# Kernel tuning notes

Measured on AMD Instinct MI355X. Metric: run time of the kernel, lower is better.

Reference implementation:

```python
import jax, jax.numpy as jnp
import numpy as np

HIDDEN = 4096
N_HEADS = 32
HEAD_DIM = HIDDEN // N_HEADS  # 128
ROPE_BASE = 10000.0


def _rotate_half(x):
    h = x.shape[-1] // 2
    return jnp.concatenate((-x[..., h:], x[..., :h]), axis=-1)


def _rope_sin_cos(position_ids):
    # position_ids: [B, S] int -> sin, cos: [B, 1, S, head_dim]
    inv_freq = 1.0 / (ROPE_BASE ** (jnp.arange(0, HEAD_DIM, 2, dtype=jnp.float32) / HEAD_DIM))
    freqs = position_ids.astype(jnp.float32)[..., None] * inv_freq  # [B,S,hd/2]
    emb = jnp.concatenate((freqs, freqs), axis=-1)  # [B,S,hd]
    return jnp.sin(emb)[:, None, :, :], jnp.cos(emb)[:, None, :, :]


def setup_inputs() -> dict:
    key = jax.random.key(0)
    k1, k2, k3 = jax.random.split(key, 3)
    B, S = 2, 2048
    hidden_states = jax.random.normal(k1, (B, S, HIDDEN), dtype=jnp.float32)
    w_qkv = jax.random.normal(k2, (HIDDEN, 3 * HIDDEN), dtype=jnp.float32) * 0.02
    wo = jax.random.normal(k3, (HIDDEN, HIDDEN), dtype=jnp.float32) * 0.02
    position_ids = jnp.broadcast_to(jnp.arange(S, dtype=jnp.int32)[None, :], (B, S))
    return {"hidden_states": hidden_states, "w_qkv": w_qkv, "wo": wo,
            "position_ids": position_ids}


def reference(hidden_states, w_qkv, wo, position_ids):
    B, S, H = hidden_states.shape
    qkv = hidden_states @ w_qkv  # [B,S,3H]
    q, k, v = jnp.split(qkv, 3, axis=-1)
    # [B,S,nH,hd] -> [B,nH,S,hd]
    q = q.reshape(B, S, N_HEADS, HEAD_DIM).transpose(0, 2, 1, 3)
    k = k.reshape(B, S, N_HEADS, HEAD_DIM).transpose(0, 2, 1, 3)
    v = v.reshape(B, S, N_HEADS, HEAD_DIM).transpose(0, 2, 1, 3)
    sin, cos = _rope_sin_cos(position_ids)  # [B,1,S,hd]
    q = q * cos + _rotate_half(q) * sin
    k = k * cos + _rotate_half(k) * sin
    scale = 1.0 / np.sqrt(HEAD_DIM)
    scores = jnp.einsum('bhqd,bhkd->bhqk', q, k) * scale
    causal = jnp.tril(jnp.ones((S, S), dtype=bool))
    scores = jnp.where(causal[None, None, :, :], scores, jnp.finfo(scores.dtype).min)
    attn = jax.nn.softmax(scores, axis=-1)
    out = jnp.einsum('bhqk,bhkd->bhqd', attn, v)  # [B,nH,S,hd]
    out = out.transpose(0, 2, 1, 3).reshape(B, S, H)
    return out @ wo
```

## Files before the change

kernel.cpp:

```cpp
#include <hip/hip_runtime.h>

typedef unsigned int u32;
typedef unsigned short u16;
typedef short short8 __attribute__((ext_vector_type(8)));
typedef float f32x4 __attribute__((ext_vector_type(4)));
typedef unsigned short us4 __attribute__((ext_vector_type(4)));

#define S_LEN 2048
#define BATCH 2
#define HID 4096
#define NH 32
#define HD 128
#define TRIH 12288

#define GCAST(p) ((const __attribute__((address_space(1))) u32*)(p))
#define LCAST(p) ((__attribute__((address_space(3))) u32*)(p))

static __device__ __forceinline__ u16 f2bf(float f) {
  union { float f; u32 u; } x; x.f = f;
  u32 u = x.u;
  u32 r = u + 0x7FFFu + ((u >> 16) & 1u);
  return (u16)(r >> 16);
}
static __device__ __forceinline__ float bf2f(u16 h) {
  union { u32 u; float f; } x; x.u = ((u32)h) << 16;
  return x.f;
}

__global__ __launch_bounds__(256) void cvt_f32_bf16(const float* __restrict__ in,
                                                    u16* __restrict__ out, int n4) {
  int i = blockIdx.x * 256 + threadIdx.x;
  if (i >= n4) return;
  float4 v = ((const float4*)in)[i];
  us4 o;
  o.x = f2bf(v.x); o.y = f2bf(v.y); o.z = f2bf(v.z); o.w = f2bf(v.w);
  ((us4*)out)[i] = o;
}

__global__ __launch_bounds__(256) void tr_cvt(const float* __restrict__ in,
                                              u16* __restrict__ out, int R, int C) {
  __shared__ float tile[64][65];
  int c0 = blockIdx.x * 64, r0 = blockIdx.y * 64;
  int tx = threadIdx.x;
  int rr = tx >> 4;
  int cc = (tx & 15) << 2;
#pragma unroll
  for (int it = 0; it < 4; ++it) {
    float4 v = *(const float4*)&in[(size_t)(r0 + rr + it * 16) * C + c0 + cc];
    tile[rr + it * 16][cc + 0] = v.x;
    tile[rr + it * 16][cc + 1] = v.y;
    tile[rr + it * 16][cc + 2] = v.z;
    tile[rr + it * 16][cc + 3] = v.w;
  }
  __syncthreads();
#pragma unroll
  for (int it = 0; it < 4; ++it) {
    int crow = rr + it * 16;
    us4 o;
    o.x = f2bf(tile[cc + 0][crow]);
    o.y = f2bf(tile[cc + 1][crow]);
    o.z = f2bf(tile[cc + 2][crow]);
    o.w = f2bf(tile[cc + 3][crow]);
    *(us4*)&out[(size_t)(c0 + crow) * R + r0 + cc] = o;
  }
}


template<int MQ, int NQ>
static __device__ __forceinline__ void mfma_quad(f32x4 (&acc)[8][4], short8 (&af)[4][2],
                                                 short8 (&bfr)[4][2]) {
#pragma unroll
  for (int ml = 0; ml < 4; ++ml)
#pragma unroll
    for (int nl = 0; nl < 2; ++nl) {
      acc[MQ*4+ml][NQ*2+nl] = __builtin_amdgcn_mfma_f32_16x16x32_bf16(
          af[ml][0], bfr[NQ*2+nl][0], acc[MQ*4+ml][NQ*2+nl], 0, 0, 0);
      acc[MQ*4+ml][NQ*2+nl] = __builtin_amdgcn_mfma_f32_16x16x32_bf16(
          af[ml][1], bfr[NQ*2+nl][1], acc[MQ*4+ml][NQ*2+nl], 0, 0, 0);
    }
}

template<int MQ>
static __device__ __forceinline__ void read_a(short8 (&af)[4][2], const u16* abase, int lane) {
#pragma unroll
  for (int ml = 0; ml < 4; ++ml) {
    int r = MQ*64 + ml*16 + (lane & 15);
#pragma unroll
    for (int kh = 0; kh < 2; ++kh) {
      int j = kh*4 + (lane >> 4);
      af[ml][kh] = *(const short8*)(abase + r*64 + ((j ^ (r & 7)) << 3));
    }
  }
}
template<int NQ>
static __device__ __forceinline__ void read_b(short8 (&bfr)[4][2], const u16* bbase,
                                              int rbase, int lane) {
#pragma unroll
  for (int nl = 0; nl < 2; ++nl) {
    int r = rbase + (NQ*2+nl)*16 + (lane & 15);
#pragma unroll
    for (int kh = 0; kh < 2; ++kh) {
      int j = kh*4 + (lane >> 4);
      bfr[NQ*2+nl][kh] = *(const short8*)(bbase + r*64 + ((j ^ (r & 7)) << 3));
    }
  }
}

#define SEAM_CLOSE0() \
  asm volatile("s_waitcnt vmcnt(0)" ::: "memory"); \
  __builtin_amdgcn_s_barrier(); \
  __builtin_amdgcn_sched_barrier(0);

template<int OUTF32>
__global__ __launch_bounds__(512, 1) void gemm256(const u16* __restrict__ A,
                                                  const u16* __restrict__ Bt,
                                                  void* __restrict__ Cout,
                                                  int M, int N, int K, int nbm) {
  __shared__ __attribute__((aligned(16))) u16 lds[65536];
  const int tid = threadIdx.x, wave = tid >> 6, lane = tid & 63;
  const int wr = wave >> 2, wc = wave & 3;
  const int nwg = gridDim.x, wg = blockIdx.x, cpx = nwg >> 3;
  const int swz = (wg & 7) * cpx + (wg >> 3);
  const size_t tileM = (size_t)(swz % nbm) * 256;
  const size_t tileN = (size_t)(swz / nbm) * 256;
  const int nIter = K >> 7;

  const int r_ = tid >> 3;
  const int gc_ = (tid & 7) ^ (r_ & 7);

  const u16* Ag = A + tileM * K;
  const u16* Bg = Bt + tileN * K;

  f32x4 acc[8][4] = {};
  short8 af[4][2], bfr[4][2];

  auto stageA = [&](int kt, int buf, int half) {
    const u16* g0 = Ag + (size_t)(half*128 + r_) * K + kt*64 + (gc_ << 3);
    u16* l = lds + buf*16384 + half*8192 + wave*512;
    __builtin_amdgcn_global_load_lds(GCAST(g0), LCAST(l), 16, 0, 0);
    __builtin_amdgcn_global_load_lds(GCAST(g0 + (size_t)64*K), LCAST(l + 4096), 16, 0, 0);
  };
  auto stageB = [&](int kt, int buf, int half) {
    const u16* g0 = Bg + (size_t)(half*128 + r_) * K + kt*64 + (gc_ << 3);
    u16* l = lds + 32768 + buf*16384 + half*8192 + wave*512;
    __builtin_amdgcn_global_load_lds(GCAST(g0), LCAST(l), 16, 0, 0);
    __builtin_amdgcn_global_load_lds(GCAST(g0 + (size_t)64*K), LCAST(l + 4096), 16, 0, 0);
  };

  const u16* a0 = lds + wr*8192;
  const u16* a1 = lds + 16384 + wr*8192;
  const u16* b0 = lds + 32768 + (wc >> 1)*8192;
  const u16* b1 = lds + 32768 + 16384 + (wc >> 1)*8192;
  const int brb = (wc & 1) * 64;

  stageA(0, 0, 0); stageA(0, 0, 1);
  stageB(0, 0, 0); stageB(0, 0, 1);
  SEAM_CLOSE0()

  for (int i = 0; i < nIter; ++i) {
    const int t1 = 2*i + 1, t2 = 2*i + 2;
    const bool more = (i + 1 < nIter);

    read_a<0>(af, a0, lane);
    read_b<0>(bfr, b0, brb, lane);
    read_b<1>(bfr, b0, brb, lane);
    stageA(t1, 1, 0); stageA(t1, 1, 1);
    stageB(t1, 1, 0); stageB(t1, 1, 1);
    mfma_quad<0, 0>(acc, af, bfr);
    mfma_quad<0, 1>(acc, af, bfr);
    read_a<1>(af, a0, lane);
    mfma_quad<1, 0>(acc, af, bfr);
    mfma_quad<1, 1>(acc, af, bfr);
    SEAM_CLOSE0()

    read_a<0>(af, a1, lane);
    read_b<0>(bfr, b1, brb, lane);
    read_b<1>(bfr, b1, brb, lane);
    if (more) { stageA(t2, 0, 0); stageA(t2, 0, 1); stageB(t2, 0, 0); stageB(t2, 0, 1); }
    mfma_quad<0, 0>(acc, af, bfr);
    mfma_quad<0, 1>(acc, af, bfr);
    read_a<1>(af, a1, lane);
    mfma_quad<1, 0>(acc, af, bfr);
    mfma_quad<1, 1>(acc, af, bfr);
    if (more) { SEAM_CLOSE0() }
  }

  const int r0o = (lane >> 4) << 2, c0o = lane & 15;
#pragma unroll
  for (int m = 0; m < 8; ++m)
#pragma unroll
    for (int n = 0; n < 4; ++n)
#pragma unroll
      for (int rr = 0; rr < 4; ++rr) {
        size_t grow = tileM + wr*128 + m*16 + r0o + rr;
        size_t gcol = tileN + wc*64 + n*16 + c0o;
        if (OUTF32) ((float*)Cout)[grow * N + gcol] = acc[m][n][rr];
        else        ((u16*)Cout)[grow * N + gcol] = f2bf(acc[m][n][rr]);
      }
}

__global__ __launch_bounds__(256) void rope_kernel(u16* __restrict__ qkv,
                                                   const int* __restrict__ pid) {
  int idx = blockIdx.x * 256 + threadIdx.x;
  int row = idx >> 9;
  int rem = idx & 511;
  int which = rem >> 8;
  int h = (rem >> 3) & 31;
  int j0 = (rem & 7) << 3;
  u16* p = qkv + (size_t)row * TRIH + which * HID + h * HD + j0;
  short8 lo = *(short8*)p;
  short8 hi = *(short8*)(p + 64);
  float pos = (float)pid[row];
  short8 olo, ohi;
#pragma unroll
  for (int i = 0; i < 8; ++i) {
    float x0 = bf2f((u16)lo[i]), x1 = bf2f((u16)hi[i]);
    float th = pos * expf(-(float)(j0 + i) * 0.14391156831212787f);
    float sn, cs;
    sincosf(th, &sn, &cs);
    olo[i] = (short)f2bf(x0 * cs - x1 * sn);
    ohi[i] = (short)f2bf(x1 * cs + x0 * sn);
  }
  *(short8*)p = olo;
  *(short8*)(p + 64) = ohi;
}

__global__ __launch_bounds__(512, 2) void attn_kernel(const u16* __restrict__ qkv,
                                                      u16* __restrict__ O) {
  const int bid = blockIdx.x;
  const int qt = 15 - (bid >> 6);
  const int bh = bid & 63;
  const int b = bh >> 5, h = bh & 31;
  const int tid = threadIdx.x, wave = tid >> 6, lane = tid & 63;
  __shared__ u16 Ks[2][64 * 128];
  __shared__ u16 VsT[2][128 * 64];
  __shared__ u16 Ps[8][16 * 64];
  const u16* base = qkv + (size_t)b * S_LEN * TRIH + h * HD;

  const int rbase = (lane >> 4) << 2;
  const int cbase = lane & 15;
  const int q_lo = qt * 128;
  const int wrow0 = q_lo + wave * 16;

  short8 qf[4];
  {
    const u16* qrow = base + (size_t)(wrow0 + cbase) * TRIH;
#pragma unroll
    for (int f = 0; f < 4; ++f)
      qf[f] = *(const short8*)(qrow + ((f * 4 + (lane >> 4)) << 3));
  }

  const int tmax_w = 2 * qt + (wave >= 4 ? 1 : 0);
  const int tmax_b = 2 * qt + 1;

  float mrun[4], lrun[4];
  f32x4 accO[8] = {};
#pragma unroll
  for (int r = 0; r < 4; ++r) { mrun[r] = -1e30f; lrun[r] = 0.f; }

  short8 kreg[2], vreg[2];
  auto load_tile = [&](int t) {
    int kv = t << 6;
#pragma unroll
    for (int it = 0; it < 2; ++it) {
      int c = tid + it * 512;
      int row = c >> 4, ch = c & 15;
      const u16* src = base + (size_t)(kv + row) * TRIH + (ch << 3);
      kreg[it] = *(const short8*)(src + HID);
      vreg[it] = *(const short8*)(src + 2 * HID);
    }
  };
  auto write_tile = [&](int buf) {
#pragma unroll
    for (int it = 0; it < 2; ++it) {
      int c = tid + it * 512;
      int row = c >> 4, ch = c & 15;
      *(short8*)(Ks[buf] + row * 128 + ((ch ^ (row & 7)) << 3)) = kreg[it];
#pragma unroll
      for (int i = 0; i < 8; ++i) {
        int d = (ch << 3) + i;
        VsT[buf][d * 64 + (((row >> 3) ^ (ch & 7)) << 3) + (row & 7)] = (u16)vreg[it][i];
      }
    }
  };

  load_tile(0);
  write_tile(0);
  load_tile(1);

  for (int t = 0; t <= tmax_b; ++t) {
    const int cur = t & 1;
    __syncthreads();
    if (t < tmax_b) write_tile(cur ^ 1);
    if (t + 2 <= tmax_b) load_tile(t + 2);

    if (t > tmax_w) continue;

    f32x4 s[4] = {};
#pragma unroll
    for (int n = 0; n < 4; ++n) {
      int krow = n * 16 + cbase;
#pragma unroll
      for (int f = 0; f < 4; ++f) {
        int ch = f * 4 + (lane >> 4);
        short8 kf = *(const short8*)(Ks[cur] + krow * 128 + ((ch ^ (krow & 7)) << 3));
        s[n] = __builtin_amdgcn_mfma_f32_16x16x32_bf16(qf[f], kf, s[n], 0, 0, 0);
      }
    }
    const float scale = 0.08838834764831845f;
    const int kv0 = t << 6;
    if (t == tmax_w) {
#pragma unroll
      for (int n = 0; n < 4; ++n)
#pragma unroll
        for (int r = 0; r < 4; ++r) {
          int kvcol = kv0 + n * 16 + cbase;
          int qrow = wrow0 + rbase + r;
          s[n][r] = (kvcol <= qrow) ? s[n][r] * scale : -1e30f;
        }
    } else {
#pragma unroll
      for (int n = 0; n < 4; ++n) s[n] *= scale;
    }

    float tmax[4];
#pragma unroll
    for (int r = 0; r < 4; ++r) {
      float tm = fmaxf(fmaxf(s[0][r], s[1][r]), fmaxf(s[2][r], s[3][r]));
      tm = fmaxf(tm, __shfl_xor(tm, 1));
      tm = fmaxf(tm, __shfl_xor(tm, 2));
      tm = fmaxf(tm, __shfl_xor(tm, 4));
      tm = fmaxf(tm, __shfl_xor(tm, 8));
      tmax[r] = tm;
    }
    bool need = false;
#pragma unroll
    for (int r = 0; r < 4; ++r) need |= (tmax[r] > mrun[r] + 8.0f);
    if (__any(need)) {
#pragma unroll
      for (int r = 0; r < 4; ++r) {
        float mnew = fmaxf(mrun[r], tmax[r]);
        float corr = __expf(mrun[r] - mnew);
        float rs = 0.f;
#pragma unroll
        for (int n = 0; n < 4; ++n) { float pv = __expf(s[n][r] - mnew); s[n][r] = pv; rs += pv; }
        rs += __shfl_xor(rs, 1); rs += __shfl_xor(rs, 2);
        rs += __shfl_xor(rs, 4); rs += __shfl_xor(rs, 8);
        lrun[r] = lrun[r] * corr + rs;
        mrun[r] = mnew;
#pragma unroll
        for (int nd = 0; nd < 8; ++nd) accO[nd][r] *= corr;
      }
    } else {
#pragma unroll
      for (int r = 0; r < 4; ++r) {
        float rs = 0.f;
#pragma unroll
        for (int n = 0; n < 4; ++n) { float pv = __expf(s[n][r] - mrun[r]); s[n][r] = pv; rs += pv; }
        rs += __shfl_xor(rs, 1); rs += __shfl_xor(rs, 2);
        rs += __shfl_xor(rs, 4); rs += __shfl_xor(rs, 8);
        lrun[r] += rs;
      }
    }

    u16* Pw = (u16*)Ps[wave];
#pragma unroll
    for (int n = 0; n < 4; ++n)
#pragma unroll
      for (int r = 0; r < 4; ++r) {
        int rl = rbase + r;
        int col = n * 16 + cbase;
        Pw[rl * 64 + (((col >> 3) ^ (rl & 7)) << 3) + (col & 7)] = f2bf(s[n][r]);
      }

    short8 pa[2];
    {
      int prow = lane & 15;
#pragma unroll
      for (int f2 = 0; f2 < 2; ++f2) {
        int ch = f2 * 4 + (lane >> 4);
        pa[f2] = *(const short8*)(Pw + prow * 64 + ((ch ^ (prow & 7)) << 3));
      }
    }
#pragma unroll
    for (int nd = 0; nd < 8; ++nd) {
      int drow = nd * 16 + cbase;
#pragma unroll
      for (int f2 = 0; f2 < 2; ++f2) {
        int ch = f2 * 4 + (lane >> 4);
        short8 vb = *(const short8*)(VsT[cur] + drow * 64 + ((ch ^ ((drow >> 3) & 7)) << 3));
        accO[nd] = __builtin_amdgcn_mfma_f32_16x16x32_bf16(pa[f2], vb, accO[nd], 0, 0, 0);
      }
    }
  }

#pragma unroll
  for (int nd = 0; nd < 8; ++nd)
#pragma unroll
    for (int r = 0; r < 4; ++r) {
      int qrow = wrow0 + rbase + r;
      int col = h * HD + nd * 16 + cbase;
      O[(size_t)(b * S_LEN + qrow) * HID + col] = f2bf(accO[nd][r] / lrun[r]);
    }
}

extern "C" void kernel_launch(void* const* d_in, const int* in_sizes, int n_in,
                              void* d_out, int out_size, void* d_ws, size_t ws_size,
                              hipStream_t stream) {
  const float* hidden = (const float*)d_in[0];
  const float* w_qkv  = (const float*)d_in[1];
  const float* wo     = (const float*)d_in[2];
  const int*   pid    = (const int*)d_in[3];

  const size_t MB = 1024ull * 1024ull;
  u16* hb    = (u16*)d_ws;
  u16* wqkvT = (u16*)((char*)d_ws + 32 * MB);
  u16* woT   = (u16*)((char*)d_ws + 128 * MB);
  u16* qkvb  = (u16*)((char*)d_ws + 160 * MB);
  u16* Obuf  = hb;

  cvt_f32_bf16<<<16384, 256, 0, stream>>>(hidden, hb, (BATCH * S_LEN * HID) / 4);
  tr_cvt<<<dim3(TRIH / 64, HID / 64), 256, 0, stream>>>(w_qkv, wqkvT, HID, TRIH);
  tr_cvt<<<dim3(HID / 64, HID / 64), 256, 0, stream>>>(wo, woT, HID, HID);

  gemm256<0><<<768, 512, 0, stream>>>(hb, wqkvT, qkvb, BATCH * S_LEN, TRIH, HID, 16);

  rope_kernel<<<(BATCH * S_LEN * 2 * NH * 8) / 256, 256, 0, stream>>>(qkvb, pid);

  attn_kernel<<<1024, 512, 0, stream>>>(qkvb, Obuf);

  gemm256<1><<<256, 512, 0, stream>>>(Obuf, woT, d_out, BATCH * S_LEN, HID, HID, 16);
}
```

Measured before the change: 823.7 us.

## Prefetch B tiles one stage earlier with partial vmcnt waits and setprio around MFMAs

Splits each GEMM half-iteration into two phases with an intermediate barrier. B tiles are now staged one sub-step ahead (t2, t3), so the seam waits use vmcnt(4) instead of draining all outstanding loads. MFMA blocks in both the GEMM and the attention kernel are wrapped in s_setprio(1)/s_setprio(0) so waves issuing matrix ops get scheduling priority. The extra barriers and the harder-to-check buffer ordering could add sync cost or expose races between LDS reads and the async global-to-LDS writes into the same buffer.

```diff
diff --git a/kernel.cpp b/kernel.cpp
--- a/kernel.cpp
+++ b/kernel.cpp
@@ -106,8 +106,12 @@
   }
 }
 
-#define SEAM_CLOSE0() \
-  asm volatile("s_waitcnt vmcnt(0)" ::: "memory"); \
+#define PHASE_CLOSE() \
+  __builtin_amdgcn_s_barrier(); \
+  __builtin_amdgcn_sched_barrier(0);
+
+#define SEAM_CLOSE(NSTR) \
+  asm volatile("s_waitcnt vmcnt(" NSTR ")" ::: "memory"); \
   __builtin_amdgcn_s_barrier(); \
   __builtin_amdgcn_sched_barrier(0);
 
@@ -155,34 +159,48 @@
 
   stageA(0, 0, 0); stageA(0, 0, 1);
   stageB(0, 0, 0); stageB(0, 0, 1);
-  SEAM_CLOSE0()
+  stageB(1, 1, 0); stageB(1, 1, 1);
+  SEAM_CLOSE("4")
 
   for (int i = 0; i < nIter; ++i) {
-    const int t1 = 2*i + 1, t2 = 2*i + 2;
+    const int t1 = 2*i + 1, t2 = 2*i + 2, t3 = 2*i + 3;
     const bool more = (i + 1 < nIter);
 
     read_a<0>(af, a0, lane);
     read_b<0>(bfr, b0, brb, lane);
     read_b<1>(bfr, b0, brb, lane);
     stageA(t1, 1, 0); stageA(t1, 1, 1);
-    stageB(t1, 1, 0); stageB(t1, 1, 1);
+    __builtin_amdgcn_s_setprio(1);
     mfma_quad<0, 0>(acc, af, bfr);
     mfma_quad<0, 1>(acc, af, bfr);
+    __builtin_amdgcn_s_setprio(0);
+    PHASE_CLOSE()
+
     read_a<1>(af, a0, lane);
+    if (more) { stageB(t2, 0, 0); stageB(t2, 0, 1); }
+    __builtin_amdgcn_s_setprio(1);
     mfma_quad<1, 0>(acc, af, bfr);
     mfma_quad<1, 1>(acc, af, bfr);
-    SEAM_CLOSE0()
+    __builtin_amdgcn_s_setprio(0);
+    if (more) { SEAM_CLOSE("4") } else { SEAM_CLOSE("0") }
 
     read_a<0>(af, a1, lane);
     read_b<0>(bfr, b1, brb, lane);
     read_b<1>(bfr, b1, brb, lane);
-    if (more) { stageA(t2, 0, 0); stageA(t2, 0, 1); stageB(t2, 0, 0); stageB(t2, 0, 1); }
+    if (more) { stageA(t2, 0, 0); stageA(t2, 0, 1); }
+    __builtin_amdgcn_s_setprio(1);
     mfma_quad<0, 0>(acc, af, bfr);
     mfma_quad<0, 1>(acc, af, bfr);
+    __builtin_amdgcn_s_setprio(0);
+    PHASE_CLOSE()
+
     read_a<1>(af, a1, lane);
+    if (more) { stageB(t3, 1, 0); stageB(t3, 1, 1); }
+    __builtin_amdgcn_s_setprio(1);
     mfma_quad<1, 0>(acc, af, bfr);
     mfma_quad<1, 1>(acc, af, bfr);
-    if (more) { SEAM_CLOSE0() }
+    __builtin_amdgcn_s_setprio(0);
+    if (more) { SEAM_CLOSE("4") } else { PHASE_CLOSE() }
   }
 
   const int r0o = (lane >> 4) << 2, c0o = lane & 15;
@@ -297,6 +315,7 @@
     if (t > tmax_w) continue;
 
     f32x4 s[4] = {};
+    __builtin_amdgcn_s_setprio(1);
 #pragma unroll
     for (int n = 0; n < 4; ++n) {
       int krow = n * 16 + cbase;
@@ -307,6 +326,7 @@
         s[n] = __builtin_amdgcn_mfma_f32_16x16x32_bf16(qf[f], kf, s[n], 0, 0, 0);
       }
     }
+    __builtin_amdgcn_s_setprio(0);
     const float scale = 0.08838834764831845f;
     const int kv0 = t << 6;
     if (t == tmax_w) {
@@ -382,6 +402,7 @@
         pa[f2] = *(const short8*)(Pw + prow * 64 + ((ch ^ (prow & 7)) << 3));
       }
     }
+    __builtin_amdgcn_s_setprio(1);
 #pragma unroll
     for (int nd = 0; nd < 8; ++nd) {
       int drow = nd * 16 + cbase;
@@ -392,6 +413,7 @@
         accO[nd] = __builtin_amdgcn_mfma_f32_16x16x32_bf16(pa[f2], vb, accO[nd], 0, 0, 0);
       }
     }
+    __builtin_amdgcn_s_setprio(0);
   }
 
 #pragma unroll
```

Result: faster. 768.1 us (-6.7%).
